# Performance work log

Hardware: AMD Instinct MI355X
Metric: run time of the kernel (lower is better)

The kernel has to match this reference:

```python
import jax, jax.numpy as jnp
import numpy as np

K, P = 20, 20  # neighbors and progressive enlargement step


def _conv1x1(w, x):  # w: (Cout, Cin), x: (B, Cin, N) -> (B, Cout, N)
    return jnp.einsum('oc,bcn->bon', w, x)


def _group_norm(x, gamma, beta, groups, eps=1e-5):  # x: (B, C, N)
    B, C, N = x.shape
    xg = x.reshape(B, groups, C // groups, N)
    m = jnp.mean(xg, axis=(2, 3), keepdims=True)
    v = jnp.var(xg, axis=(2, 3), keepdims=True)
    xn = ((xg - m) * jax.lax.rsqrt(v + eps)).reshape(B, C, N)
    return xn * gamma[None, :, None] + beta[None, :, None]


def _block(x, w, g, b, groups):  # Conv1d(k=1) + GroupNorm + LeakyReLU(0.2)
    h = _group_norm(_conv1x1(w, x), g, b, groups)
    return jnp.where(h > 0, h, 0.2 * h)


def _gather_max(f, idx):  # f: (B, C, N), idx: (B, N, k) -> (B, C, N)
    ft = jnp.swapaxes(f, 1, 2)  # (B, N, C)
    g = jax.vmap(lambda ff, ii: ff[ii])(ft, idx)  # (B, N, k, C)
    return jnp.swapaxes(jnp.max(g, axis=2), 1, 2)


def _forward(x,
             w1a, g1a, b1a, w1b, g1b, b1b,
             w2a, g2a, b2a, w2b, g2b, b2b,
             w3a, g3a, b3a, w3b, g3b, b3b,
             w4a, g4a, b4a, w4b, g4b, b4b,
             w5_1, g5_1, b5_1, w5_2, g5_2, b5_2):
    xc = jnp.swapaxes(x, 1, 2)  # (B, C, N)
    # knn_acc: negative squared pairwise distance, take top-(k+3P)
    xx = jnp.sum(xc * xc, axis=1, keepdims=True)  # (B, 1, N)
    inner = jnp.einsum('bcn,bcm->bnm', xc, xc)  # (B, N, N)
    pd = 2.0 * inner - jnp.swapaxes(xx, 1, 2) - xx  # -||xi-xj||^2
    _, idx_pool = jax.lax.top_k(pd, K + 3 * P)  # (B, N, k+3P)

    def layer(xin, wa, ga, ba, wb, gb, bb, groups, idx):
        fa = _block(xin, wa, ga, ba, groups)
        fb = _block(xin, wb, gb, bb, groups)
        return _gather_max(fa, idx) + fb

    x1 = layer(xc, w1a, g1a, b1a, w1b, g1b, b1b, 8, idx_pool[:, :, :K])
    x2 = layer(x1, w2a, g2a, b2a, w2b, g2b, b2b, 8, idx_pool[:, :, :K + P])
    x3 = layer(x2, w3a, g3a, b3a, w3b, g3b, b3b, 8, idx_pool[:, :, :K + 2 * P])
    x4 = layer(x3, w4a, g4a, b4a, w4b, g4b, b4b, 16, idx_pool)
    x_cat = jnp.concatenate([x1, x2, x3, x4], axis=1)  # (B, 512, N)
    h = _block(x_cat, w5_1, g5_1, b5_1, 16)  # (B, 1024, N)
    h = _block(h, w5_2, g5_2, b5_2, 16)      # (B, 512, N)
    return jnp.swapaxes(h, 1, 2)  # (B, N, 512)


def setup_inputs() -> dict:
    key = jax.random.key(0)
    ks = iter(jax.random.split(key, 16))
    d = {"x": jax.random.normal(next(ks), (8, 2048, 3), dtype=jnp.float32)}

    def add(name, cout, cin):
        d["w" + name] = jax.random.normal(next(ks), (cout, cin), dtype=jnp.float32) * 0.1
        d["g" + name] = jnp.ones((cout,), dtype=jnp.float32)
        d["b" + name] = jnp.zeros((cout,), dtype=jnp.float32)

    add("1a", 64, 3); add("1b", 64, 3)
    add("2a", 64, 64); add("2b", 64, 64)
    add("3a", 128, 64); add("3b", 128, 64)
    add("4a", 256, 128); add("4b", 256, 128)
    add("5_1", 1024, 512); add("5_2", 512, 1024)
    return d


def reference(x,
              w1a, g1a, b1a, w1b, g1b, b1b,
              w2a, g2a, b2a, w2b, g2b, b2b,
              w3a, g3a, b3a, w3b, g3b, b3b,
              w4a, g4a, b4a, w4b, g4b, b4b,
              w5_1, g5_1, b5_1, w5_2, g5_2, b5_2):
    return _forward(x,
                    w1a, g1a, b1a, w1b, g1b, b1b,
                    w2a, g2a, b2a, w2b, g2b, b2b,
                    w3a, g3a, b3a, w3b, g3b, b3b,
                    w4a, g4a, b4a, w4b, g4b, b4b,
                    w5_1, g5_1, b5_1, w5_2, g5_2, b5_2)
```

## Files before the change

### kernel.cpp

```cpp
#include <hip/hip_runtime.h>
#include <stdint.h>

typedef unsigned short u16;
typedef unsigned int u32;
typedef unsigned long long u64;
typedef __attribute__((ext_vector_type(8))) __bf16 bf16x8;
typedef __attribute__((ext_vector_type(8))) u16 u16x8;
typedef __attribute__((ext_vector_type(4))) float f32x4;

#define DEVI __device__ __forceinline__

DEVI u16 f2bf(float f) {
  u32 u = __float_as_uint(f);
  u += 0x7FFFu + ((u >> 16) & 1u);
  return (u16)(u >> 16);
}
DEVI float bf2f(u16 h) { return __uint_as_float(((u32)h) << 16); }
DEVI u16 mono(u16 b) {
  return (b & 0x8000u) ? (u16)~b : (u16)(b | 0x8000u);
}
DEVI u16 unmono(u16 t) {
  return (t & 0x8000u) ? (u16)(t ^ 0x8000u) : (u16)(~t);
}

DEVI void glds16(const void* g, void* l) {
  __builtin_amdgcn_global_load_lds((const __attribute__((address_space(1))) void*)g,
                                   (__attribute__((address_space(3))) void*)l, 16, 0, 0);
}

__global__ void k_zero(float* __restrict__ p, int n) {
  int i = blockIdx.x * 256 + threadIdx.x;
  if (i < n) p[i] = 0.f;
}

__global__ void k_pack_coords(const float* __restrict__ x, float4* __restrict__ c4) {
  int g = blockIdx.x * 256 + threadIdx.x;
  float x0 = x[g*3], x1 = x[g*3+1], x2 = x[g*3+2];
  float n = __fadd_rn(__fadd_rn(__fmul_rn(x0,x0), __fmul_rn(x1,x1)), __fmul_rn(x2,x2));
  c4[g] = make_float4(x0, x1, x2, n);
}

__global__ void k_pack_w(const float* __restrict__ w2a, const float* __restrict__ w2b,
                         const float* __restrict__ w3a, const float* __restrict__ w3b,
                         const float* __restrict__ w4a, const float* __restrict__ w4b,
                         const float* __restrict__ w51, const float* __restrict__ w52,
                         u16* __restrict__ wbf) {
  int g = blockIdx.x * 256 + threadIdx.x;
  const float* s; int off;
  if      (g <    4096) { s = w2a; off = g; }
  else if (g <    8192) { s = w2b; off = g - 4096; }
  else if (g <   16384) { s = w3a; off = g - 8192; }
  else if (g <   24576) { s = w3b; off = g - 16384; }
  else if (g <   57344) { s = w4a; off = g - 24576; }
  else if (g <   90112) { s = w4b; off = g - 57344; }
  else if (g <  614400) { s = w51; off = g - 90112; }
  else                  { s = w52; off = g - 614400; }
  wbf[g] = f2bf(s[off]);
}

__global__ __launch_bounds__(256) void k_knn(const float4* __restrict__ c4, int* __restrict__ idxp) {
  __shared__ u64 cand[4][128];
  const int wid = threadIdx.x >> 6;
  const int lane = threadIdx.x & 63;
  const int batch = blockIdx.x & 7;
  const int qib = (blockIdx.x >> 3) * 4 + wid;
  const int blk = (batch << 11) + qib;
  const float4* cb = c4 + (batch << 11);
  const float4 q = cb[qib];

  u32 key[32];
  #pragma unroll
  for (int s = 0; s < 32; ++s) {
    float4 c = cb[s*64 + lane];
    float inner = __fadd_rn(__fadd_rn(__fmul_rn(q.x,c.x), __fmul_rn(q.y,c.y)), __fmul_rn(q.z,c.z));
    float pd = __fsub_rn(__fsub_rn(__fmul_rn(2.0f, inner), q.w), c.w);
    u32 bits = __float_as_uint(pd);
    key[s] = (bits & 0x80000000u) ? ~bits : (bits | 0x80000000u);
  }

  u32 T = 0;
  for (int bit = 30; bit >= 0; --bit) {
    u32 Tc = T | (1u << bit);
    int c = 0;
    #pragma unroll
    for (int s = 0; s < 32; ++s)
      c += __popcll(__ballot(key[s] >= Tc));
    if (c >= 80) { T = Tc; if (c <= 128) break; }
  }

  cand[wid][lane] = 0ull;
  cand[wid][lane + 64] = 0ull;
  asm volatile("s_waitcnt lgkmcnt(0)" ::: "memory");

  const u64 below = (lane == 0) ? 0ull : (~0ull >> (64 - lane));
  int base = 0;
  #pragma unroll
  for (int s = 0; s < 32; ++s) {
    u64 msk = __ballot(key[s] >= T);
    if (key[s] >= T) {
      int pos = base + (int)__popcll(msk & below);
      if (pos < 128)
        cand[wid][pos] = (((u64)key[s]) << 32) | (u32)(2047 - (s*64 + lane));
    }
    base += (int)__popcll(msk);
  }
  asm volatile("s_waitcnt lgkmcnt(0)" ::: "memory");

  u64 v0 = cand[wid][lane];
  u64 v1 = cand[wid][lane + 64];
  #pragma unroll
  for (int k2 = 2; k2 <= 128; k2 <<= 1) {
    #pragma unroll
    for (int j = k2 >> 1; j > 0; j >>= 1) {
      if (j == 64) {
        u64 mx = v0 > v1 ? v0 : v1;
        u64 mn = v0 > v1 ? v1 : v0;
        v0 = mx; v1 = mn;
      } else {
        u64 p0 = __shfl_xor(v0, j, 64);
        u64 p1 = __shfl_xor(v1, j, 64);
        bool lowlane = ((lane & j) == 0);
        bool d0 = ((lane & k2) == 0);
        bool d1 = (((lane + 64) & k2) == 0);
        bool wm0 = (d0 == lowlane);
        bool wm1 = (d1 == lowlane);
        u64 mx0 = v0 > p0 ? v0 : p0, mn0 = v0 > p0 ? p0 : v0;
        u64 mx1 = v1 > p1 ? v1 : p1, mn1 = v1 > p1 ? p1 : v1;
        v0 = wm0 ? mx0 : mn0;
        v1 = wm1 ? mx1 : mn1;
      }
    }
  }

  idxp[blk*80 + lane] = 2047 - (int)(u32)v0;
  if (lane < 16) idxp[blk*80 + 64 + lane] = 2047 - (int)(u32)v1;
}

__global__ __launch_bounds__(256) void k_conv1(const float* __restrict__ x,
    const float* __restrict__ w1a, const float* __restrict__ w1b,
    const float* __restrict__ g1a, const float* __restrict__ g1b,
    u16* __restrict__ out, float* __restrict__ gsum) {
  __shared__ float xs[384];
  __shared__ float colsum[128], colss[128];
  const int tid = threadIdx.x;
  const int P0 = blockIdx.x * 128;
  for (int i = tid; i < 384; i += 256) xs[i] = x[P0*3 + i];
  if (tid < 128) { colsum[tid] = 0.f; colss[tid] = 0.f; }
  __syncthreads();

  const int c = tid & 127;
  const int half = tid >> 7;
  const float* w = (c < 64) ? (w1a + 3*c) : (w1b + 3*(c-64));
  float wx = w[0], wy = w[1], wz = w[2];
  float gam = (c < 64) ? g1a[c] : g1b[c-64];
  u16 flip = (gam < 0.f) ? (u16)0xFFFF : (u16)0;

  float s = 0.f, ss = 0.f;
  #pragma unroll 4
  for (int p_ = 0; p_ < 64; ++p_) {
    int p = (half << 6) + p_;
    float h = wx*xs[p*3] + wy*xs[p*3+1] + wz*xs[p*3+2];
    s += h; ss += h*h;
    out[(size_t)(P0 + p)*128 + c] = (u16)(mono(f2bf(h)) ^ flip);
  }
  atomicAdd(&colsum[c], s);
  atomicAdd(&colss[c], ss);
  __syncthreads();
  if (tid < 16) {
    float gs = 0.f, gss = 0.f;
    #pragma unroll
    for (int q = 0; q < 8; ++q) { gs += colsum[tid*8+q]; gss += colss[tid*8+q]; }
    int b = blockIdx.x >> 4;
    atomicAdd(&gsum[(b*16 + tid)*2],   gs);
    atomicAdd(&gsum[(b*16 + tid)*2+1], gss);
  }
}

__global__ __launch_bounds__(256) void k_gather(const u16* __restrict__ conv, int Ctot, int Ca,
    int CgShift, int NG, const float* __restrict__ gsum,
    const float* __restrict__ ga, const float* __restrict__ ba,
    const float* __restrict__ gb, const float* __restrict__ bb,
    const int* __restrict__ idxp, int k,
    u16* __restrict__ xcat, int outOff, int lppShift) {
  const int batch = blockIdx.x & 7;
  const int blkin = blockIdx.x >> 3;
  const int lgid = blkin * 256 + threadIdx.x;
  const int p_in = lgid >> lppShift;
  const int c8 = (lgid & ((1 << lppShift) - 1)) * 8;
  const int p = (batch << 11) + p_in;
  const int* irow = idxp + (size_t)p * 80;
  const u16* cb = conv + ((size_t)(batch << 11)) * Ctot + c8;

  const int gia = c8 >> CgShift;
  const int gib = (Ca + c8) >> CgShift;
  const float cnt = (float)(2048 << CgShift);
  float2 sa = *(const float2*)(gsum + (size_t)(batch*NG + gia)*2);
  float2 sb = *(const float2*)(gsum + (size_t)(batch*NG + gib)*2);
  float meanA = sa.x / cnt, rstdA = rsqrtf(sa.y / cnt - meanA*meanA + 1e-5f);
  float meanB = sb.x / cnt, rstdB = rsqrtf(sb.y / cnt - meanB*meanB + 1e-5f);

  float gav[8], bav[8], gbv[8], bbv[8];
  *(float4*)&gav[0] = *(const float4*)(ga + c8); *(float4*)&gav[4] = *(const float4*)(ga + c8 + 4);
  *(float4*)&bav[0] = *(const float4*)(ba + c8); *(float4*)&bav[4] = *(const float4*)(ba + c8 + 4);
  *(float4*)&gbv[0] = *(const float4*)(gb + c8); *(float4*)&gbv[4] = *(const float4*)(gb + c8 + 4);
  *(float4*)&bbv[0] = *(const float4*)(bb + c8); *(float4*)&bbv[4] = *(const float4*)(bb + c8 + 4);

  u16x8 fbv = *(const u16x8*)(conv + (size_t)p * Ctot + Ca + c8);

  u16x8 m8 = (u16x8)(u16)0;
  for (int j0 = 0; j0 < k; j0 += 4) {
    int4 mi4 = *(const int4*)(irow + j0);
    int mis[4] = {mi4.x, mi4.y, mi4.z, mi4.w};
    u16x8 rows[4];
    #pragma unroll
    for (int u = 0; u < 4; ++u)
      rows[u] = *(const u16x8*)(cb + (size_t)mis[u] * Ctot);
    #pragma unroll
    for (int u = 0; u < 4; ++u)
      m8 = __builtin_elementwise_max(m8, rows[u]);
  }

  u16 ov[8];
  #pragma unroll
  for (int q = 0; q < 8; ++q) {
    u16 fA = (gav[q] < 0.f) ? (u16)0xFFFF : (u16)0;
    u16 fB = (gbv[q] < 0.f) ? (u16)0xFFFF : (u16)0;
    float xa = bf2f(unmono((u16)((u16)m8[q] ^ fA)));
    float ha = (xa - meanA) * rstdA * gav[q] + bav[q];
    ha = ha > 0.f ? ha : 0.2f * ha;
    float xb = bf2f(unmono((u16)((u16)fbv[q] ^ fB)));
    float hb = (xb - meanB) * rstdB * gbv[q] + bbv[q];
    hb = hb > 0.f ? hb : 0.2f * hb;
    ov[q] = f2bf(ha + hb);
  }
  *(u16x8*)(xcat + (size_t)p * 512 + outOff + c8) = *(u16x8*)ov;
}

__global__ __launch_bounds__(256) void k_apply51(u16* __restrict__ act,
    const float* __restrict__ gsum, const float* __restrict__ g, const float* __restrict__ b) {
  int gid = blockIdx.x * 256 + threadIdx.x;
  size_t e = (size_t)gid * 8;
  int row = (int)(e >> 10);
  int c = (int)e & 1023;
  int grp = c >> 6;
  float2 s = *(const float2*)(gsum + (size_t)((row >> 11)*16 + grp)*2);
  const float cnt = 131072.f;
  float mean = s.x / cnt, rstd = rsqrtf(s.y / cnt - mean*mean + 1e-5f);
  uint4 v = *(const uint4*)(act + e);
  u32 vv[4] = {v.x, v.y, v.z, v.w};
  #pragma unroll
  for (int q2 = 0; q2 < 4; ++q2) {
    int c0 = c + q2*2, c1 = c0 + 1;
    float x0 = bf2f((u16)(vv[q2] & 0xFFFF));
    float x1 = bf2f((u16)(vv[q2] >> 16));
    float h0 = (x0 - mean) * rstd * g[c0] + b[c0];
    float h1 = (x1 - mean) * rstd * g[c1] + b[c1];
    h0 = h0 > 0.f ? h0 : 0.2f * h0;
    h1 = h1 > 0.f ? h1 : 0.2f * h1;
    vv[q2] = (u32)f2bf(h0) | (((u32)f2bf(h1)) << 16);
  }
  *(uint4*)(act + e) = make_uint4(vv[0], vv[1], vv[2], vv[3]);
}

__global__ __launch_bounds__(256) void k_apply52(float* __restrict__ act,
    const float* __restrict__ gsum, const float* __restrict__ g, const float* __restrict__ b) {
  int gid = blockIdx.x * 256 + threadIdx.x;
  size_t e = (size_t)gid * 4;
  int row = (int)(e >> 9);
  int c = (int)e & 511;
  int grp = c >> 5;
  float2 s = *(const float2*)(gsum + (size_t)((row >> 11)*16 + grp)*2);
  const float cnt = 65536.f;
  float mean = s.x / cnt, rstd = rsqrtf(s.y / cnt - mean*mean + 1e-5f);
  float4 v = *(const float4*)(act + e);
  float h[4] = {v.x, v.y, v.z, v.w};
  #pragma unroll
  for (int q = 0; q < 4; ++q) {
    float o = (h[q] - mean) * rstd * g[c+q] + b[c+q];
    h[q] = o > 0.f ? o : 0.2f * o;
  }
  *(float4*)(act + e) = make_float4(h[0], h[1], h[2], h[3]);
}

template<int OUTF32, int MONO>
__global__ __launch_bounds__(256) void k_gemm(const u16* __restrict__ A, int lda,
    const u16* __restrict__ Bw, int K, void* __restrict__ outp, int ldc,
    int CgShift, int NG, float* __restrict__ gsum,
    const float* __restrict__ ga, const float* __restrict__ gb, int Ca) {
  constexpr int BK = 64;
  __shared__ __align__(16) u16 As[128 * BK];
  __shared__ __align__(16) u16 Bs[128 * BK];
  __shared__ float colsum[128], colss[128];
  const int tid = threadIdx.x;
  const int wid = tid >> 6, lane = tid & 63;
  const int tileM = blockIdx.x * 128, tileN = blockIdx.y * 128;
  const int wm = wid >> 1, wn = wid & 1;
  const int lr = lane & 15, lk = (lane >> 4) * 8;
  f32x4 acc[4][4] = {};
  for (int k0 = 0; k0 < K; k0 += BK) {
    __syncthreads();
    #pragma unroll
    for (int i = 0; i < 4; ++i) {
      int flat = i * 256 + tid;
      int row = flat >> 3, ck = flat & 7;
      glds16(A + (size_t)(tileM + row) * lda + (k0 + ck * 8), (char*)As + flat * 16);
    }
    #pragma unroll
    for (int i = 0; i < 4; ++i) {
      int flat = i * 256 + tid;
      int row = flat >> 3, ck = flat & 7;
      glds16(Bw + (size_t)(tileN + row) * K + (k0 + ck * 8), (char*)Bs + flat * 16);
    }
    __syncthreads();
    #pragma unroll
    for (int ks = 0; ks < 2; ++ks) {
      bf16x8 af[4], bfr[4];
      #pragma unroll
      for (int i = 0; i < 4; ++i)
        af[i] = *(const bf16x8*)&As[(wm*64 + i*16 + lr) * BK + ks*32 + lk];
      #pragma unroll
      for (int j = 0; j < 4; ++j)
        bfr[j] = *(const bf16x8*)&Bs[(wn*64 + j*16 + lr) * BK + ks*32 + lk];
      #pragma unroll
      for (int i = 0; i < 4; ++i)
        #pragma unroll
        for (int j = 0; j < 4; ++j)
          acc[i][j] = __builtin_amdgcn_mfma_f32_16x16x32_bf16(af[i], bfr[j], acc[i][j], 0, 0, 0);
    }
  }
  const int orow0 = tileM + wm*64 + ((lane >> 4) * 4);
  const int ocol0 = tileN + wn*64 + lr;

  u16 flip[4] = {0,0,0,0};
  if (MONO) {
    #pragma unroll
    for (int j = 0; j < 4; ++j) {
      int colg = ocol0 + j*16;
      float gm = (colg < Ca) ? ga[colg] : gb[colg - Ca];
      flip[j] = (gm < 0.f) ? (u16)0xFFFF : (u16)0;
    }
  }

  float csum[4] = {0.f,0.f,0.f,0.f}, css[4] = {0.f,0.f,0.f,0.f};
  #pragma unroll
  for (int i = 0; i < 4; ++i)
    #pragma unroll
    for (int j = 0; j < 4; ++j)
      #pragma unroll
      for (int r = 0; r < 4; ++r) {
        int row = orow0 + i*16 + r;
        int col = ocol0 + j*16;
        float v = acc[i][j][r];
        csum[j] += v; css[j] += v*v;
        if (OUTF32) ((float*)outp)[(size_t)row * ldc + col] = v;
        else {
          u16 st = f2bf(v);
          if (MONO) st = (u16)(mono(st) ^ flip[j]);
          ((u16*)outp)[(size_t)row * ldc + col] = st;
        }
      }

  #pragma unroll
  for (int mask = 16; mask <= 32; mask <<= 1)
    #pragma unroll
    for (int j = 0; j < 4; ++j) {
      csum[j] += __shfl_xor(csum[j], mask, 64);
      css[j]  += __shfl_xor(css[j],  mask, 64);
    }
  if (tid < 128) { colsum[tid] = 0.f; colss[tid] = 0.f; }
  __syncthreads();
  if ((lane >> 4) == 0) {
    #pragma unroll
    for (int j = 0; j < 4; ++j) {
      int col = wn*64 + j*16 + lr;
      atomicAdd(&colsum[col], csum[j]);
      atomicAdd(&colss[col],  css[j]);
    }
  }
  __syncthreads();
  const int NGtile = 128 >> CgShift;
  if (tid < NGtile) {
    float s = 0.f, ss = 0.f;
    const int Cg = 1 << CgShift;
    for (int c0 = tid << CgShift; c0 < (tid << CgShift) + Cg; ++c0) { s += colsum[c0]; ss += colss[c0]; }
    int b = tileM >> 11;
    int gidx = (tileN >> CgShift) + tid;
    atomicAdd(&gsum[(size_t)(b*NG + gidx)*2],   s);
    atomicAdd(&gsum[(size_t)(b*NG + gidx)*2+1], ss);
  }
}

extern "C" void kernel_launch(void* const* d_in, const int* in_sizes, int n_in,
                              void* d_out, int out_size, void* d_ws, size_t ws_size,
                              hipStream_t stream) {
  const float* x   = (const float*)d_in[0];
  const float* w1a = (const float*)d_in[1];
  const float* g1a = (const float*)d_in[2];
  const float* b1a = (const float*)d_in[3];
  const float* w1b = (const float*)d_in[4];
  const float* g1b = (const float*)d_in[5];
  const float* b1b = (const float*)d_in[6];
  const float* w2a = (const float*)d_in[7];
  const float* g2a = (const float*)d_in[8];
  const float* b2a = (const float*)d_in[9];
  const float* w2b = (const float*)d_in[10];
  const float* g2b = (const float*)d_in[11];
  const float* b2b = (const float*)d_in[12];
  const float* w3a = (const float*)d_in[13];
  const float* g3a = (const float*)d_in[14];
  const float* b3a = (const float*)d_in[15];
  const float* w3b = (const float*)d_in[16];
  const float* g3b = (const float*)d_in[17];
  const float* b3b = (const float*)d_in[18];
  const float* w4a = (const float*)d_in[19];
  const float* g4a = (const float*)d_in[20];
  const float* b4a = (const float*)d_in[21];
  const float* w4b = (const float*)d_in[22];
  const float* g4b = (const float*)d_in[23];
  const float* b4b = (const float*)d_in[24];
  const float* w51 = (const float*)d_in[25];
  const float* g51 = (const float*)d_in[26];
  const float* b51 = (const float*)d_in[27];
  const float* w52 = (const float*)d_in[28];
  const float* g52 = (const float*)d_in[29];
  const float* b52 = (const float*)d_in[30];

  char* ws = (char*)d_ws;
  int*    idxp   = (int*)   (ws + 0);
  float4* c4     = (float4*)(ws + 5242880);
  u16*    wbf    = (u16*)   (ws + 5505024);
  float*  gsum   = (float*) (ws + 7782400);
  u16*    convAB = (u16*)   (ws + 7790592);
  u16*    h1     = (u16*)   (ws + 24567808);
  u16*    xcat   = (u16*)   (ws + 58122240);
  u16* wc2 = wbf, *wc3 = wbf + 8192, *wc4 = wbf + 24576;
  u16* w51b = wbf + 90112, *w52b = wbf + 614400;
  float* outf = (float*)d_out;
  float* gsL1 = gsum;        float* gsL2 = gsum + 256;  float* gsL3 = gsum + 512;
  float* gsL4 = gsum + 768;  float* gs51 = gsum + 1280; float* gs52 = gsum + 1536;

  k_zero<<<7, 256, 0, stream>>>(gsum, 1792);
  k_pack_coords<<<64, 256, 0, stream>>>(x, c4);
  k_pack_w<<<4448, 256, 0, stream>>>(w2a, w2b, w3a, w3b, w4a, w4b, w51, w52, wbf);
  k_knn<<<4096, 256, 0, stream>>>(c4, idxp);

  k_conv1<<<128, 256, 0, stream>>>(x, w1a, w1b, g1a, g1b, convAB, gsL1);
  k_gather<<<512, 256, 0, stream>>>(convAB, 128, 64, 3, 16, gsL1,
                                    g1a, b1a, g1b, b1b, idxp, 20, xcat, 0, 3);

  k_gemm<0,1><<<dim3(128,1), 256, 0, stream>>>(xcat + 0, 512, wc2, 64, convAB, 128,
                                               3, 16, gsL2, g2a, g2b, 64);
  k_gather<<<512, 256, 0, stream>>>(convAB, 128, 64, 3, 16, gsL2,
                                    g2a, b2a, g2b, b2b, idxp, 40, xcat, 64, 3);

  k_gemm<0,1><<<dim3(128,2), 256, 0, stream>>>(xcat + 64, 512, wc3, 64, convAB, 256,
                                               4, 16, gsL3, g3a, g3b, 128);
  k_gather<<<1024, 256, 0, stream>>>(convAB, 256, 128, 4, 16, gsL3,
                                     g3a, b3a, g3b, b3b, idxp, 60, xcat, 128, 4);

  k_gemm<0,1><<<dim3(128,4), 256, 0, stream>>>(xcat + 128, 512, wc4, 128, convAB, 512,
                                               4, 32, gsL4, g4a, g4b, 256);
  k_gather<<<2048, 256, 0, stream>>>(convAB, 512, 256, 4, 32, gsL4,
                                     g4a, b4a, g4b, b4b, idxp, 80, xcat, 256, 5);

  k_gemm<0,0><<<dim3(128,8), 256, 0, stream>>>(xcat, 512, w51b, 512, h1, 1024,
                                               6, 16, gs51, g51, g51, 1024);
  k_apply51<<<8192, 256, 0, stream>>>(h1, gs51, g51, b51);

  k_gemm<1,0><<<dim3(128,4), 256, 0, stream>>>(h1, 1024, w52b, 1024, (void*)outf, 512,
                                               5, 16, gs52, g52, g52, 512);
  k_apply52<<<8192, 256, 0, stream>>>(outf, gs52, g52, b52);
}
```

Before: 280.6 us.

## Radix-4 threshold search, rank-based top-k sort, fold gsum zeroing into pack kernel

The kNN threshold search now settles two bits per iteration by counting three candidate thresholds at once, which halves the serial loop trips. The 128-element bitonic shuffle sort is replaced by a rank computation: each lane counts how many LDS candidates beat its two entries and writes them straight to their output slot. The separate zeroing kernel is merged into the coordinate-pack kernel, saving one launch. The rank approach does 128 LDS reads per lane instead of shuffles, and the radix-4 search does three ballots per key per step.

```diff
diff --git a/kernel.cpp b/kernel.cpp
--- a/kernel.cpp
+++ b/kernel.cpp
@@ -28,13 +28,10 @@
                                    (__attribute__((address_space(3))) void*)l, 16, 0, 0);
 }
 
-__global__ void k_zero(float* __restrict__ p, int n) {
-  int i = blockIdx.x * 256 + threadIdx.x;
-  if (i < n) p[i] = 0.f;
-}
-
-__global__ void k_pack_coords(const float* __restrict__ x, float4* __restrict__ c4) {
+__global__ void k_pack_coords(const float* __restrict__ x, float4* __restrict__ c4,
+                              float* __restrict__ gsum) {
   int g = blockIdx.x * 256 + threadIdx.x;
+  if (g < 1792) gsum[g] = 0.f;
   float x0 = x[g*3], x1 = x[g*3+1], x2 = x[g*3+2];
   float n = __fadd_rn(__fadd_rn(__fmul_rn(x0,x0), __fmul_rn(x1,x1)), __fmul_rn(x2,x2));
   c4[g] = make_float4(x0, x1, x2, n);
@@ -79,13 +76,22 @@
   }
 
   u32 T = 0;
-  for (int bit = 30; bit >= 0; --bit) {
-    u32 Tc = T | (1u << bit);
-    int c = 0;
-    #pragma unroll
-    for (int s = 0; s < 32; ++s)
-      c += __popcll(__ballot(key[s] >= Tc));
-    if (c >= 80) { T = Tc; if (c <= 128) break; }
+  for (int bit = 31; bit >= 1; bit -= 2) {
+    u32 T01 = T | (1u << (bit - 1));
+    u32 T10 = T | (2u << (bit - 1));
+    u32 T11 = T | (3u << (bit - 1));
+    int c11 = 0, c10 = 0, c01 = 0;
+    #pragma unroll
+    for (int s = 0; s < 32; ++s) {
+      c11 += __popcll(__ballot(key[s] >= T11));
+      c10 += __popcll(__ballot(key[s] >= T10));
+      c01 += __popcll(__ballot(key[s] >= T01));
+    }
+    int c = -1;
+    if (c11 >= 80)      { T = T11; c = c11; }
+    else if (c10 >= 80) { T = T10; c = c10; }
+    else if (c01 >= 80) { T = T01; c = c01; }
+    if (c >= 80 && c <= 128) break;
   }
 
   cand[wid][lane] = 0ull;
@@ -106,34 +112,17 @@
   }
   asm volatile("s_waitcnt lgkmcnt(0)" ::: "memory");
 
-  u64 v0 = cand[wid][lane];
-  u64 v1 = cand[wid][lane + 64];
-  #pragma unroll
-  for (int k2 = 2; k2 <= 128; k2 <<= 1) {
-    #pragma unroll
-    for (int j = k2 >> 1; j > 0; j >>= 1) {
-      if (j == 64) {
-        u64 mx = v0 > v1 ? v0 : v1;
-        u64 mn = v0 > v1 ? v1 : v0;
-        v0 = mx; v1 = mn;
-      } else {
-        u64 p0 = __shfl_xor(v0, j, 64);
-        u64 p1 = __shfl_xor(v1, j, 64);
-        bool lowlane = ((lane & j) == 0);
-        bool d0 = ((lane & k2) == 0);
-        bool d1 = (((lane + 64) & k2) == 0);
-        bool wm0 = (d0 == lowlane);
-        bool wm1 = (d1 == lowlane);
-        u64 mx0 = v0 > p0 ? v0 : p0, mn0 = v0 > p0 ? p0 : v0;
-        u64 mx1 = v1 > p1 ? v1 : p1, mn1 = v1 > p1 ? p1 : v1;
-        v0 = wm0 ? mx0 : mn0;
-        v1 = wm1 ? mx1 : mn1;
-      }
-    }
-  }
-
-  idxp[blk*80 + lane] = 2047 - (int)(u32)v0;
-  if (lane < 16) idxp[blk*80 + 64 + lane] = 2047 - (int)(u32)v1;
+  u64 e0 = cand[wid][lane];
+  u64 e1 = cand[wid][lane + 64];
+  int r0 = 0, r1 = 0;
+  #pragma unroll 16
+  for (int f = 0; f < 128; ++f) {
+    u64 v = cand[wid][f];
+    r0 += (v > e0) ? 1 : 0;
+    r1 += (v > e1) ? 1 : 0;
+  }
+  if (r0 < 80) idxp[(size_t)blk*80 + r0] = 2047 - (int)(u32)e0;
+  if (r1 < 80) idxp[(size_t)blk*80 + r1] = 2047 - (int)(u32)e1;
 }
 
 __global__ __launch_bounds__(256) void k_conv1(const float* __restrict__ x,
@@ -439,8 +428,7 @@
   float* gsL1 = gsum;        float* gsL2 = gsum + 256;  float* gsL3 = gsum + 512;
   float* gsL4 = gsum + 768;  float* gs51 = gsum + 1280; float* gs52 = gsum + 1536;
 
-  k_zero<<<7, 256, 0, stream>>>(gsum, 1792);
-  k_pack_coords<<<64, 256, 0, stream>>>(x, c4);
+  k_pack_coords<<<64, 256, 0, stream>>>(x, c4, gsum);
   k_pack_w<<<4448, 256, 0, stream>>>(w2a, w2b, w3a, w3b, w4a, w4b, w51, w52, wbf);
   k_knn<<<4096, 256, 0, stream>>>(c4, idxp);
 
```

New measurement: 290.7 us. 3.6% more time.

## Fuse GroupNorm+LeakyReLU of conv5_1 into the A-tile load of conv5_2 GEMM

Applied to the files above, without the earlier changes.

Removes the standalone elementwise pass over the bf16 h1 activation (16M elements read and written). A small kernel now precomputes per-batch, per-channel scale and bias, and the second GEMM applies normalize plus LeakyReLU while loading A tiles through registers into LDS. The trade-off is that those tiles lose the direct global-to-LDS async load and pay for extra ALU work and scale/bias loads. The separate gsum zeroing kernel is also folded into the coordinate-pack kernel, saving one launch.

```diff
diff --git a/kernel.cpp b/kernel.cpp
--- a/kernel.cpp
+++ b/kernel.cpp
@@ -28,13 +28,10 @@
                                    (__attribute__((address_space(3))) void*)l, 16, 0, 0);
 }
 
-__global__ void k_zero(float* __restrict__ p, int n) {
-  int i = blockIdx.x * 256 + threadIdx.x;
-  if (i < n) p[i] = 0.f;
-}
-
-__global__ void k_pack_coords(const float* __restrict__ x, float4* __restrict__ c4) {
+__global__ void k_pack_coords(const float* __restrict__ x, float4* __restrict__ c4,
+                              float* __restrict__ gsum) {
   int g = blockIdx.x * 256 + threadIdx.x;
+  if (g < 1792) gsum[g] = 0.f;
   float x0 = x[g*3], x1 = x[g*3+1], x2 = x[g*3+2];
   float n = __fadd_rn(__fadd_rn(__fmul_rn(x0,x0), __fmul_rn(x1,x1)), __fmul_rn(x2,x2));
   c4[g] = make_float4(x0, x1, x2, n);
@@ -132,8 +129,8 @@
     }
   }
 
-  idxp[blk*80 + lane] = 2047 - (int)(u32)v0;
-  if (lane < 16) idxp[blk*80 + 64 + lane] = 2047 - (int)(u32)v1;
+  idxp[(size_t)blk*80 + lane] = 2047 - (int)(u32)v0;
+  if (lane < 16) idxp[(size_t)blk*80 + 64 + lane] = 2047 - (int)(u32)v1;
 }
 
 __global__ __launch_bounds__(256) void k_conv1(const float* __restrict__ x,
@@ -236,30 +233,18 @@
   *(u16x8*)(xcat + (size_t)p * 512 + outOff + c8) = *(u16x8*)ov;
 }
 
-__global__ __launch_bounds__(256) void k_apply51(u16* __restrict__ act,
-    const float* __restrict__ gsum, const float* __restrict__ g, const float* __restrict__ b) {
-  int gid = blockIdx.x * 256 + threadIdx.x;
-  size_t e = (size_t)gid * 8;
-  int row = (int)(e >> 10);
-  int c = (int)e & 1023;
+__global__ void k_sb51(const float* __restrict__ gsum, const float* __restrict__ g,
+                       const float* __restrict__ b, float* __restrict__ sc,
+                       float* __restrict__ bi) {
+  int i = blockIdx.x * 256 + threadIdx.x;
+  int bb = i >> 10, c = i & 1023;
   int grp = c >> 6;
-  float2 s = *(const float2*)(gsum + (size_t)((row >> 11)*16 + grp)*2);
-  const float cnt = 131072.f;
-  float mean = s.x / cnt, rstd = rsqrtf(s.y / cnt - mean*mean + 1e-5f);
-  uint4 v = *(const uint4*)(act + e);
-  u32 vv[4] = {v.x, v.y, v.z, v.w};
-  #pragma unroll
-  for (int q2 = 0; q2 < 4; ++q2) {
-    int c0 = c + q2*2, c1 = c0 + 1;
-    float x0 = bf2f((u16)(vv[q2] & 0xFFFF));
-    float x1 = bf2f((u16)(vv[q2] >> 16));
-    float h0 = (x0 - mean) * rstd * g[c0] + b[c0];
-    float h1 = (x1 - mean) * rstd * g[c1] + b[c1];
-    h0 = h0 > 0.f ? h0 : 0.2f * h0;
-    h1 = h1 > 0.f ? h1 : 0.2f * h1;
-    vv[q2] = (u32)f2bf(h0) | (((u32)f2bf(h1)) << 16);
-  }
-  *(uint4*)(act + e) = make_uint4(vv[0], vv[1], vv[2], vv[3]);
+  float2 s = *(const float2*)(gsum + (size_t)(bb*16 + grp)*2);
+  float mean = s.x / 131072.f;
+  float rstd = rsqrtf(s.y / 131072.f - mean*mean + 1e-5f);
+  float A = rstd * g[c];
+  sc[i] = A;
+  bi[i] = b[c] - mean * A;
 }
 
 __global__ __launch_bounds__(256) void k_apply52(float* __restrict__ act,
@@ -282,11 +267,12 @@
   *(float4*)(act + e) = make_float4(h[0], h[1], h[2], h[3]);
 }
 
-template<int OUTF32, int MONO>
+template<int OUTF32, int MONO, int TRANSA>
 __global__ __launch_bounds__(256) void k_gemm(const u16* __restrict__ A, int lda,
     const u16* __restrict__ Bw, int K, void* __restrict__ outp, int ldc,
     int CgShift, int NG, float* __restrict__ gsum,
-    const float* __restrict__ ga, const float* __restrict__ gb, int Ca) {
+    const float* __restrict__ ga, const float* __restrict__ gb, int Ca,
+    const float* __restrict__ scA, const float* __restrict__ biA) {
   constexpr int BK = 64;
   __shared__ __align__(16) u16 As[128 * BK];
   __shared__ __align__(16) u16 Bs[128 * BK];
@@ -296,6 +282,8 @@
   const int tileM = blockIdx.x * 128, tileN = blockIdx.y * 128;
   const int wm = wid >> 1, wn = wid & 1;
   const int lr = lane & 15, lk = (lane >> 4) * 8;
+  const float* scb = TRANSA ? (scA + (size_t)(tileM >> 11) * 1024) : nullptr;
+  const float* bib = TRANSA ? (biA + (size_t)(tileM >> 11) * 1024) : nullptr;
   f32x4 acc[4][4] = {};
   for (int k0 = 0; k0 < K; k0 += BK) {
     __syncthreads();
@@ -303,7 +291,31 @@
     for (int i = 0; i < 4; ++i) {
       int flat = i * 256 + tid;
       int row = flat >> 3, ck = flat & 7;
-      glds16(A + (size_t)(tileM + row) * lda + (k0 + ck * 8), (char*)As + flat * 16);
+      if (TRANSA) {
+        int cbase = k0 + ck * 8;
+        uint4 v = *(const uint4*)(A + (size_t)(tileM + row) * lda + cbase);
+        float4 s0 = *(const float4*)(scb + cbase);
+        float4 s1 = *(const float4*)(scb + cbase + 4);
+        float4 b0 = *(const float4*)(bib + cbase);
+        float4 b1 = *(const float4*)(bib + cbase + 4);
+        float sc8[8] = {s0.x,s0.y,s0.z,s0.w,s1.x,s1.y,s1.z,s1.w};
+        float bi8[8] = {b0.x,b0.y,b0.z,b0.w,b1.x,b1.y,b1.z,b1.w};
+        u32 vv[4] = {v.x, v.y, v.z, v.w};
+        u32 ov[4];
+        #pragma unroll
+        for (int q2 = 0; q2 < 4; ++q2) {
+          float x0 = bf2f((u16)(vv[q2] & 0xFFFF));
+          float x1 = bf2f((u16)(vv[q2] >> 16));
+          float o0 = x0 * sc8[q2*2]   + bi8[q2*2];
+          float o1 = x1 * sc8[q2*2+1] + bi8[q2*2+1];
+          o0 = o0 > 0.f ? o0 : 0.2f * o0;
+          o1 = o1 > 0.f ? o1 : 0.2f * o1;
+          ov[q2] = (u32)f2bf(o0) | (((u32)f2bf(o1)) << 16);
+        }
+        *(uint4*)((char*)As + flat * 16) = make_uint4(ov[0], ov[1], ov[2], ov[3]);
+      } else {
+        glds16(A + (size_t)(tileM + row) * lda + (k0 + ck * 8), (char*)As + flat * 16);
+      }
     }
     #pragma unroll
     for (int i = 0; i < 4; ++i) {
@@ -433,14 +445,15 @@
   u16*    convAB = (u16*)   (ws + 7790592);
   u16*    h1     = (u16*)   (ws + 24567808);
   u16*    xcat   = (u16*)   (ws + 58122240);
+  float*  sc51   = (float*) (ws + 7790592);
+  float*  bi51   = (float*) (ws + 7823360);
   u16* wc2 = wbf, *wc3 = wbf + 8192, *wc4 = wbf + 24576;
   u16* w51b = wbf + 90112, *w52b = wbf + 614400;
   float* outf = (float*)d_out;
   float* gsL1 = gsum;        float* gsL2 = gsum + 256;  float* gsL3 = gsum + 512;
   float* gsL4 = gsum + 768;  float* gs51 = gsum + 1280; float* gs52 = gsum + 1536;
 
-  k_zero<<<7, 256, 0, stream>>>(gsum, 1792);
-  k_pack_coords<<<64, 256, 0, stream>>>(x, c4);
+  k_pack_coords<<<64, 256, 0, stream>>>(x, c4, gsum);
   k_pack_w<<<4448, 256, 0, stream>>>(w2a, w2b, w3a, w3b, w4a, w4b, w51, w52, wbf);
   k_knn<<<4096, 256, 0, stream>>>(c4, idxp);
 
@@ -448,26 +461,26 @@
   k_gather<<<512, 256, 0, stream>>>(convAB, 128, 64, 3, 16, gsL1,
                                     g1a, b1a, g1b, b1b, idxp, 20, xcat, 0, 3);
 
-  k_gemm<0,1><<<dim3(128,1), 256, 0, stream>>>(xcat + 0, 512, wc2, 64, convAB, 128,
-                                               3, 16, gsL2, g2a, g2b, 64);
+  k_gemm<0,1,0><<<dim3(128,1), 256, 0, stream>>>(xcat + 0, 512, wc2, 64, convAB, 128,
+                                                 3, 16, gsL2, g2a, g2b, 64, nullptr, nullptr);
   k_gather<<<512, 256, 0, stream>>>(convAB, 128, 64, 3, 16, gsL2,
                                     g2a, b2a, g2b, b2b, idxp, 40, xcat, 64, 3);
 
-  k_gemm<0,1><<<dim3(128,2), 256, 0, stream>>>(xcat + 64, 512, wc3, 64, convAB, 256,
-                                               4, 16, gsL3, g3a, g3b, 128);
+  k_gemm<0,1,0><<<dim3(128,2), 256, 0, stream>>>(xcat + 64, 512, wc3, 64, convAB, 256,
+                                                 4, 16, gsL3, g3a, g3b, 128, nullptr, nullptr);
   k_gather<<<1024, 256, 0, stream>>>(convAB, 256, 128, 4, 16, gsL3,
                                      g3a, b3a, g3b, b3b, idxp, 60, xcat, 128, 4);
 
-  k_gemm<0,1><<<dim3(128,4), 256, 0, stream>>>(xcat + 128, 512, wc4, 128, convAB, 512,
-                                               4, 32, gsL4, g4a, g4b, 256);
+  k_gemm<0,1,0><<<dim3(128,4), 256, 0, stream>>>(xcat + 128, 512, wc4, 128, convAB, 512,
+                                                 4, 32, gsL4, g4a, g4b, 256, nullptr, nullptr);
   k_gather<<<2048, 256, 0, stream>>>(convAB, 512, 256, 4, 32, gsL4,
                                      g4a, b4a, g4b, b4b, idxp, 80, xcat, 256, 5);
 
-  k_gemm<0,0><<<dim3(128,8), 256, 0, stream>>>(xcat, 512, w51b, 512, h1, 1024,
-                                               6, 16, gs51, g51, g51, 1024);
-  k_apply51<<<8192, 256, 0, stream>>>(h1, gs51, g51, b51);
-
-  k_gemm<1,0><<<dim3(128,4), 256, 0, stream>>>(h1, 1024, w52b, 1024, (void*)outf, 512,
-                                               5, 16, gs52, g52, g52, 512);
+  k_gemm<0,0,0><<<dim3(128,8), 256, 0, stream>>>(xcat, 512, w51b, 512, h1, 1024,
+                                                 6, 16, gs51, g51, g51, 1024, nullptr, nullptr);
+  k_sb51<<<32, 256, 0, stream>>>(gs51, g51, b51, sc51, bi51);
+
+  k_gemm<1,0,1><<<dim3(128,4), 256, 0, stream>>>(h1, 1024, w52b, 1024, (void*)outf, 512,
+                                                 5, 16, gs52, g52, g52, 512, sc51, bi51);
   k_apply52<<<8192, 256, 0, stream>>>(outf, gs52, g52, b52);
 }
```

Result: faster. 273.4 us (-2.6%).
